# Optimization experiments

Hardware: AMD Instinct MI355X
Metric: run time of the kernel (lower is better)

Reference implementation:

```python
import jax, jax.numpy as jnp
import numpy as np

N_NODES, N_EDGES, HIDDEN, N_GRAPHS = 100000, 500000, 128, 2048
ATOM_DIM, BOND_DIM, OUT_DIM = 4, 3, 1


def setup_inputs() -> dict:
    key = jax.random.key(0)
    ks = jax.random.split(key, 13)
    s = 0.05  # small init scale to keep relu+scatter depth iterations numerically tame
    return {
        "x": jax.random.normal(ks[0], (N_NODES, ATOM_DIM), jnp.float32),
        "edge_index": jax.random.randint(ks[1], (2, N_EDGES), 0, N_NODES, dtype=jnp.int32),
        "edge_attr": jax.random.normal(ks[2], (N_EDGES, BOND_DIM), jnp.float32),
        "batch": jnp.sort(jax.random.randint(ks[3], (N_NODES,), 0, N_GRAPHS, dtype=jnp.int32)),
        "depth": 3,
        # DMPNN weights (bias=False)
        "W_i": jax.random.normal(ks[4], (HIDDEN, ATOM_DIM + BOND_DIM), jnp.float32) * s,
        "W_m": jax.random.normal(ks[5], (HIDDEN, HIDDEN), jnp.float32) * s,
        "W_a": jax.random.normal(ks[6], (HIDDEN, ATOM_DIM + HIDDEN), jnp.float32) * s,
        # FFN: Linear(d,4d) -> relu -> dropout(eval=identity) -> Linear(4d,d)
        "W1": jax.random.normal(ks[7], (4 * HIDDEN, HIDDEN), jnp.float32) * s,
        "b1": jnp.zeros((4 * HIDDEN,), jnp.float32),
        "W2": jax.random.normal(ks[8], (HIDDEN, 4 * HIDDEN), jnp.float32) * s,
        "b2": jnp.zeros((HIDDEN,), jnp.float32),
        "W_last": jax.random.normal(ks[9], (OUT_DIM, HIDDEN), jnp.float32) * s,
        "b_last": jnp.zeros((OUT_DIM,), jnp.float32),
    }


def reference(x, edge_index, edge_attr, batch, depth, W_i, W_m, W_a, W1, b1, W2, b2, W_last, b_last):
    src, dst = edge_index[0], edge_index[1]
    E = edge_attr.shape[0]
    N = x.shape[0]
    # h: per-edge state [E, H]
    h = jax.nn.relu(jnp.concatenate([x[src], edge_attr], axis=1) @ W_i.T)
    for _ in range(depth):
        # message: relu(W_m h) gathered at src, scatter-add to dst; PyG infers
        # dim_size from h (edge-level here), so aggregation buffer has E rows.
        m = jax.nn.relu(h @ W_m.T)
        h = h + jax.ops.segment_sum(m[src], dst, num_segments=E)
    # index_add_ edge states to nodes
    node_emb = jax.ops.segment_sum(h, dst, num_segments=N)  # [N, H]
    node_emb = jax.nn.relu(jnp.concatenate([x, node_emb], axis=1) @ W_a.T)
    # global_add_pool over graphs
    g = jax.ops.segment_sum(node_emb, batch, num_segments=N_GRAPHS)  # [G, H]
    g = jax.nn.relu(g @ W1.T + b1) @ W2.T + b2  # FFN (dropout eval = identity)
    return g @ W_last.T + b_last  # [G, OUT_DIM]
```

## Files before the change

kernel.cpp:

```cpp
#include <hip/hip_runtime.h>


#define NN 100000
#define NE 500000
#define HID 128
#define NG 2048
#define NB_SCAN 391

typedef __attribute__((ext_vector_type(8))) short bf16x8;
typedef __attribute__((ext_vector_type(4))) float f32x4;

__device__ __forceinline__ float b2f(ushort u) {
  return __uint_as_float(((uint)u) << 16);
}
__device__ __forceinline__ ushort f2b(float f) {
  uint u = __float_as_uint(f);
  return (ushort)((u + 0x7FFF + ((u >> 16) & 1)) >> 16);
}

__global__ __launch_bounds__(256) void k_convw(const float* __restrict__ Wm,
    const float* __restrict__ Wa, ushort* __restrict__ wmb, ushort* __restrict__ wab) {
  int i = blockIdx.x * 256 + threadIdx.x;
  if (i >= HID * HID) return;
  wmb[i] = f2b(Wm[i]);
  int c = i >> 7, k = i & 127;
  wab[i] = f2b(Wa[c * 132 + 4 + k]);
}

__global__ __launch_bounds__(256) void k_init_h(const int* __restrict__ src,
    const float* __restrict__ x, const float* __restrict__ ea,
    const float* __restrict__ Wi, ushort* __restrict__ h) {
  __shared__ float wis[HID * 7];
  for (int i = threadIdx.x; i < HID * 7; i += 256) wis[i] = Wi[i];
  __syncthreads();
  int idx = blockIdx.x * 256 + threadIdx.x;
  int e = idx >> 7, c = idx & 127;
  if (e >= NN) return;
  int s = src[e];
  const float* w = &wis[c * 7];
  float acc = x[s*4+0]*w[0] + x[s*4+1]*w[1] + x[s*4+2]*w[2] + x[s*4+3]*w[3]
            + ea[e*3+0]*w[4] + ea[e*3+1]*w[5] + ea[e*3+2]*w[6];
  h[(size_t)e * HID + c] = f2b(fmaxf(acc, 0.f));
}

__global__ __launch_bounds__(256) void k_hist(const int* __restrict__ dst,
                                              int* __restrict__ cnt) {
  int e = blockIdx.x * 256 + threadIdx.x;
  if (e < NE) atomicAdd(&cnt[dst[e]], 1);
}

__global__ __launch_bounds__(256) void k_scan1(const int* __restrict__ cnt,
    int* __restrict__ outp, int* __restrict__ bsums) {
  __shared__ int s[256];
  int t = threadIdx.x;
  int i = blockIdx.x * 256 + t;
  int v = (i < NN) ? cnt[i] : 0;
  s[t] = v;
  __syncthreads();
  for (int off = 1; off < 256; off <<= 1) {
    int u = (t >= off) ? s[t - off] : 0;
    __syncthreads();
    s[t] += u;
    __syncthreads();
  }
  if (i < NN) outp[i] = s[t] - v;
  if (t == 255) bsums[blockIdx.x] = s[255];
}

__global__ __launch_bounds__(512) void k_scan2(int* __restrict__ bsums) {
  __shared__ int s[512];
  int t = threadIdx.x;
  int v = (t < NB_SCAN) ? bsums[t] : 0;
  s[t] = v;
  __syncthreads();
  for (int off = 1; off < 512; off <<= 1) {
    int u = (t >= off) ? s[t - off] : 0;
    __syncthreads();
    s[t] += u;
    __syncthreads();
  }
  if (t < NB_SCAN) bsums[t] = s[t] - v;
}

__global__ __launch_bounds__(256) void k_scan3(int* __restrict__ outp,
                                               const int* __restrict__ bsums) {
  int i = blockIdx.x * 256 + threadIdx.x;
  if (i < NN) outp[i] += bsums[blockIdx.x];
  if (i == 0) outp[NN] = NE;
}

__global__ __launch_bounds__(256) void k_fill(const int* __restrict__ src,
    const int* __restrict__ dst, const int* __restrict__ rowptr,
    int* __restrict__ cursor, int* __restrict__ csr_src, int* __restrict__ csr_eid) {
  int e = blockIdx.x * 256 + threadIdx.x;
  if (e >= NE) return;
  int d = dst[e];
  int pos = atomicAdd(&cursor[d], 1);
  int o = rowptr[d] + pos;
  csr_src[o] = src[e];
  csr_eid[o] = e;
}

__global__ __launch_bounds__(256) void k_goff(const int* __restrict__ batch,
                                              int* __restrict__ goff) {
  int g = blockIdx.x * 256 + threadIdx.x;
  if (g > NG) return;
  int lo = 0, hi = NN;
  while (lo < hi) { int mid = (lo + hi) >> 1; if (batch[mid] < g) lo = mid + 1; else hi = mid; }
  goff[g] = lo;
}

template <bool HASX>
__global__ __launch_bounds__(256) void k_mfma(const ushort* __restrict__ A,
    const ushort* __restrict__ Wb, const float* __restrict__ X,
    const float* __restrict__ WaF, ushort* __restrict__ O, int nrows) {
  int tid = threadIdx.x;
  int wave = tid >> 6;
  int lane = tid & 63;
  int wr = wave >> 1, wc = wave & 1;
  int row0 = blockIdx.x * 64 + wr * 32;
  int col0 = wc * 64;
  int l15 = lane & 15, l4 = lane >> 4;

  f32x4 acc[2][4];
#pragma unroll
  for (int mi = 0; mi < 2; ++mi)
#pragma unroll
    for (int ni = 0; ni < 4; ++ni) acc[mi][ni] = (f32x4){0.f, 0.f, 0.f, 0.f};

  if (HASX) {
    float4 wv[4];
#pragma unroll
    for (int ni = 0; ni < 4; ++ni)
      wv[ni] = *reinterpret_cast<const float4*>(&WaF[(size_t)(col0 + ni * 16 + l15) * 132]);
#pragma unroll
    for (int mi = 0; mi < 2; ++mi)
#pragma unroll
      for (int j = 0; j < 4; ++j) {
        int r = row0 + mi * 16 + l4 * 4 + j;
        if (r < nrows) {
          float4 xv = *reinterpret_cast<const float4*>(&X[(size_t)r * 4]);
#pragma unroll
          for (int ni = 0; ni < 4; ++ni)
            acc[mi][ni][j] = xv.x * wv[ni].x + xv.y * wv[ni].y
                           + xv.z * wv[ni].z + xv.w * wv[ni].w;
        }
      }
  }

  const bf16x8 zero8 = {0, 0, 0, 0, 0, 0, 0, 0};
#pragma unroll
  for (int k0 = 0; k0 < HID; k0 += 32) {
    bf16x8 a[2], b[4];
#pragma unroll
    for (int mi = 0; mi < 2; ++mi) {
      int r = row0 + mi * 16 + l15;
      a[mi] = (r < nrows)
            ? *reinterpret_cast<const bf16x8*>(&A[(size_t)r * HID + k0 + l4 * 8])
            : zero8;
    }
#pragma unroll
    for (int ni = 0; ni < 4; ++ni) {
      int c = col0 + ni * 16 + l15;
      b[ni] = *reinterpret_cast<const bf16x8*>(&Wb[(size_t)c * HID + k0 + l4 * 8]);
    }
#pragma unroll
    for (int mi = 0; mi < 2; ++mi)
#pragma unroll
      for (int ni = 0; ni < 4; ++ni)
        acc[mi][ni] = __builtin_amdgcn_mfma_f32_16x16x32_bf16(a[mi], b[ni], acc[mi][ni], 0, 0, 0);
  }

#pragma unroll
  for (int mi = 0; mi < 2; ++mi)
#pragma unroll
    for (int j = 0; j < 4; ++j) {
      int r = row0 + mi * 16 + l4 * 4 + j;
      if (r >= nrows) continue;
#pragma unroll
      for (int ni = 0; ni < 4; ++ni) {
        int c = col0 + ni * 16 + l15;
        O[(size_t)r * HID + c] = f2b(fmaxf(acc[mi][ni][j], 0.f));
      }
    }
}

__global__ __launch_bounds__(256) void k_gather_add(const ushort* __restrict__ m,
    const int* __restrict__ rowptr, const int* __restrict__ csr_src,
    ushort* __restrict__ h) {
  int idx = blockIdx.x * 256 + threadIdx.x;
  int n = idx >> 5;
  if (n >= NN) return;
  int c4 = (idx & 31) << 2;
  int beg = rowptr[n], end = rowptr[n + 1];
  float a0 = 0.f, a1 = 0.f, a2 = 0.f, a3 = 0.f;
  for (int i = beg; i < end; ++i) {
    int s = csr_src[i];
    ushort4 v = *reinterpret_cast<const ushort4*>(&m[(size_t)s * HID + c4]);
    a0 += b2f(v.x); a1 += b2f(v.y); a2 += b2f(v.z); a3 += b2f(v.w);
  }
  ushort* p = &h[(size_t)n * HID + c4];
  ushort4 hv = *reinterpret_cast<const ushort4*>(p);
  ushort4 o;
  o.x = f2b(b2f(hv.x) + a0); o.y = f2b(b2f(hv.y) + a1);
  o.z = f2b(b2f(hv.z) + a2); o.w = f2b(b2f(hv.w) + a3);
  *reinterpret_cast<ushort4*>(p) = o;
}

__global__ __launch_bounds__(256) void k_node_agg(const ushort* __restrict__ h,
    const int* __restrict__ rowptr, const int* __restrict__ csr_src,
    const int* __restrict__ csr_eid, const float* __restrict__ x,
    const float* __restrict__ ea, const float* __restrict__ Wi,
    ushort* __restrict__ ne) {
  int idx = blockIdx.x * 256 + threadIdx.x;
  int n = idx >> 5;
  int c4 = (idx & 31) << 2;
  float w[4][7];
#pragma unroll
  for (int j = 0; j < 4; ++j)
#pragma unroll
    for (int k = 0; k < 7; ++k) w[j][k] = Wi[(c4 + j) * 7 + k];
  if (n >= NN) return;
  int beg = rowptr[n], end = rowptr[n + 1];
  float a0 = 0.f, a1 = 0.f, a2 = 0.f, a3 = 0.f;
  for (int i = beg; i < end; ++i) {
    int e = csr_eid[i];
    if (e < NN) {
      ushort4 v = *reinterpret_cast<const ushort4*>(&h[(size_t)e * HID + c4]);
      a0 += b2f(v.x); a1 += b2f(v.y); a2 += b2f(v.z); a3 += b2f(v.w);
    } else {
      int s = csr_src[i];
      float4 xv = *reinterpret_cast<const float4*>(&x[(size_t)s * 4]);
      float e0 = ea[(size_t)e*3+0], e1 = ea[(size_t)e*3+1], e2 = ea[(size_t)e*3+2];
      a0 += fmaxf(xv.x*w[0][0]+xv.y*w[0][1]+xv.z*w[0][2]+xv.w*w[0][3]+e0*w[0][4]+e1*w[0][5]+e2*w[0][6], 0.f);
      a1 += fmaxf(xv.x*w[1][0]+xv.y*w[1][1]+xv.z*w[1][2]+xv.w*w[1][3]+e0*w[1][4]+e1*w[1][5]+e2*w[1][6], 0.f);
      a2 += fmaxf(xv.x*w[2][0]+xv.y*w[2][1]+xv.z*w[2][2]+xv.w*w[2][3]+e0*w[2][4]+e1*w[2][5]+e2*w[2][6], 0.f);
      a3 += fmaxf(xv.x*w[3][0]+xv.y*w[3][1]+xv.z*w[3][2]+xv.w*w[3][3]+e0*w[3][4]+e1*w[3][5]+e2*w[3][6], 0.f);
    }
  }
  ushort4 o;
  o.x = f2b(a0); o.y = f2b(a1); o.z = f2b(a2); o.w = f2b(a3);
  *reinterpret_cast<ushort4*>(&ne[(size_t)n * HID + c4]) = o;
}

__global__ __launch_bounds__(256) void k_pool(const ushort* __restrict__ na,
    const int* __restrict__ goff, float* __restrict__ g) {
  int idx = blockIdx.x * 256 + threadIdx.x;
  int gid = idx >> 5;
  if (gid >= NG) return;
  int c4 = (idx & 31) << 2;
  int beg = goff[gid], end = goff[gid + 1];
  float a0 = 0.f, a1 = 0.f, a2 = 0.f, a3 = 0.f;
  for (int n = beg; n < end; ++n) {
    ushort4 v = *reinterpret_cast<const ushort4*>(&na[(size_t)n * HID + c4]);
    a0 += b2f(v.x); a1 += b2f(v.y); a2 += b2f(v.z); a3 += b2f(v.w);
  }
  *reinterpret_cast<float4*>(&g[(size_t)gid * HID + c4]) = make_float4(a0, a1, a2, a3);
}

template <bool RELU>
__global__ __launch_bounds__(256) void k_gemm64(const float* __restrict__ A,
    const float* __restrict__ W, const float* __restrict__ bias,
    float* __restrict__ O, int nrows, int K, int N) {
  __shared__ float As[64][33];
  __shared__ float Bs[32][68];
  int tid = threadIdx.x;
  int row0 = blockIdx.x * 64;
  int col0 = blockIdx.y * 64;
  int tn = tid & 15;
  int tm = tid >> 4;
  float acc[4][4];
#pragma unroll
  for (int i = 0; i < 4; ++i)
#pragma unroll
    for (int j = 0; j < 4; ++j) acc[i][j] = 0.f;

  for (int k0 = 0; k0 < K; k0 += 32) {
    int ar = tid >> 3;
    int ak = (tid & 7) << 2;
#pragma unroll
    for (int rr = 0; rr < 2; ++rr) {
      int r = row0 + ar + rr * 32;
      float4 v = make_float4(0.f, 0.f, 0.f, 0.f);
      if (r < nrows) v = *reinterpret_cast<const float4*>(&A[(size_t)r * K + k0 + ak]);
      As[ar + rr*32][ak+0] = v.x; As[ar + rr*32][ak+1] = v.y;
      As[ar + rr*32][ak+2] = v.z; As[ar + rr*32][ak+3] = v.w;
    }
    int c = tid & 63;
    int kq = tid >> 6;
#pragma unroll
    for (int it = 0; it < 2; ++it) {
      int kk = kq * 4 + it * 16;
      float4 v = *reinterpret_cast<const float4*>(&W[(size_t)(col0 + c) * K + k0 + kk]);
      Bs[kk+0][c] = v.x; Bs[kk+1][c] = v.y; Bs[kk+2][c] = v.z; Bs[kk+3][c] = v.w;
    }
    __syncthreads();
#pragma unroll 8
    for (int k = 0; k < 32; ++k) {
      float av[4];
#pragma unroll
      for (int i = 0; i < 4; ++i) av[i] = As[tm*4 + i][k];
      float4 bv = *reinterpret_cast<const float4*>(&Bs[k][tn*4]);
#pragma unroll
      for (int i = 0; i < 4; ++i) {
        acc[i][0] = fmaf(av[i], bv.x, acc[i][0]);
        acc[i][1] = fmaf(av[i], bv.y, acc[i][1]);
        acc[i][2] = fmaf(av[i], bv.z, acc[i][2]);
        acc[i][3] = fmaf(av[i], bv.w, acc[i][3]);
      }
    }
    __syncthreads();
  }
#pragma unroll
  for (int i = 0; i < 4; ++i) {
    int r = row0 + tm * 4 + i;
    if (r >= nrows) continue;
    float4 o;
    int c = col0 + tn * 4;
    o.x = acc[i][0] + bias[c+0];
    o.y = acc[i][1] + bias[c+1];
    o.z = acc[i][2] + bias[c+2];
    o.w = acc[i][3] + bias[c+3];
    if (RELU) {
      o.x = fmaxf(o.x, 0.f); o.y = fmaxf(o.y, 0.f);
      o.z = fmaxf(o.z, 0.f); o.w = fmaxf(o.w, 0.f);
    }
    *reinterpret_cast<float4*>(&O[(size_t)r * N + c]) = o;
  }
}

__global__ __launch_bounds__(256) void k_last(const float* __restrict__ g3,
    const float* __restrict__ Wl, const float* __restrict__ bl,
    float* __restrict__ out) {
  int wid = (blockIdx.x * 256 + threadIdx.x) >> 6;
  int lane = threadIdx.x & 63;
  if (wid >= NG) return;
  float a = g3[(size_t)wid*128 + lane] * Wl[lane]
          + g3[(size_t)wid*128 + 64 + lane] * Wl[64 + lane];
  for (int off = 32; off; off >>= 1) a += __shfl_down(a, off);
  if (lane == 0) out[wid] = a + bl[0];
}

extern "C" void kernel_launch(void* const* d_in, const int* in_sizes, int n_in,
                              void* d_out, int out_size, void* d_ws, size_t ws_size,
                              hipStream_t stream) {
  const float* x    = (const float*)d_in[0];
  const int*   eidx = (const int*)d_in[1];
  const float* ea   = (const float*)d_in[2];
  const int*   batch= (const int*)d_in[3];
  const float* Wi   = (const float*)d_in[5];
  const float* Wm   = (const float*)d_in[6];
  const float* Wa   = (const float*)d_in[7];
  const float* W1   = (const float*)d_in[8];
  const float* b1   = (const float*)d_in[9];
  const float* W2   = (const float*)d_in[10];
  const float* b2   = (const float*)d_in[11];
  const float* Wl   = (const float*)d_in[12];
  const float* bl   = (const float*)d_in[13];
  float* out = (float*)d_out;

  const int* src = eidx;
  const int* dst = eidx + NE;

  char* p = (char*)d_ws;
  ushort* hb  = (ushort*)p; p += (size_t)NN * HID * 2;
  ushort* mb  = (ushort*)p; p += (size_t)NN * HID * 2;
  ushort* wmb = (ushort*)p; p += (size_t)HID * HID * 2;
  ushort* wab = (ushort*)p; p += (size_t)HID * HID * 2;
  float* g  = (float*)p; p += (size_t)NG * 128 * 4;
  float* g2 = (float*)p; p += (size_t)NG * 512 * 4;
  float* g3 = (float*)p; p += (size_t)NG * 128 * 4;
  int* rowptr = (int*)p; p += (size_t)(NN + 4) * 4;
  int* cursor = (int*)p; p += (size_t)NN * 4;
  int* bsums  = (int*)p; p += 512 * 4;
  int* goff   = (int*)p; p += (size_t)(NG + 4) * 4;
  int* csr_src= (int*)p; p += (size_t)NE * 4;
  int* csr_eid= (int*)p; p += (size_t)NE * 4;

  hipMemsetAsync(rowptr, 0, (size_t)(NN + 4 + NN) * sizeof(int), stream);
  k_hist <<<(NE + 255) / 256, 256, 0, stream>>>(dst, rowptr);
  k_scan1<<<NB_SCAN, 256, 0, stream>>>(rowptr, cursor, bsums);
  k_scan2<<<1, 512, 0, stream>>>(bsums);
  k_scan3<<<NB_SCAN, 256, 0, stream>>>(cursor, bsums);
  int* rp  = cursor;
  int* cur = rowptr;
  hipMemsetAsync(cur, 0, (size_t)NN * sizeof(int), stream);
  k_fill <<<(NE + 255) / 256, 256, 0, stream>>>(src, dst, rp, cur, csr_src, csr_eid);
  k_goff <<<(NG + 256) / 256, 256, 0, stream>>>(batch, goff);

  k_convw<<<(HID * HID + 255) / 256, 256, 0, stream>>>(Wm, Wa, wmb, wab);

  k_init_h<<<(NN * HID) / 256, 256, 0, stream>>>(src, x, ea, Wi, hb);

  int gemm_grid = (NN + 63) / 64;
  for (int it = 0; it < 3; ++it) {
    k_mfma<false><<<gemm_grid, 256, 0, stream>>>(hb, wmb, nullptr, nullptr, mb, NN);
    k_gather_add<<<(NN * 32 + 255) / 256, 256, 0, stream>>>(mb, rp, csr_src, hb);
  }

  k_node_agg<<<(NN * 32 + 255) / 256, 256, 0, stream>>>(hb, rp, csr_src, csr_eid,
                                                        x, ea, Wi, mb);
  k_mfma<true><<<gemm_grid, 256, 0, stream>>>(mb, wab, x, Wa, hb, NN);

  k_pool<<<(NG * 32 + 255) / 256, 256, 0, stream>>>(hb, goff, g);

  dim3 grid1((NG + 63) / 64, 512 / 64);
  k_gemm64<true><<<grid1, 256, 0, stream>>>(g, W1, b1, g2, NG, 128, 512);
  dim3 grid2((NG + 63) / 64, 128 / 64);
  k_gemm64<false><<<grid2, 256, 0, stream>>>(g2, W2, b2, g3, NG, 512, 128);
  k_last<<<(NG * 64) / 256, 256, 0, stream>>>(g3, Wl, bl, out);
}
```

Baseline: 502.9 us.

## Fuse gather-add into MFMA GEMM via LDS staging and pack CSR as int2

The scatter/gather-add of each depth iteration is fused with the next W_m GEMM: each block gathers neighbour messages for its 64 rows, updates h, writes the bf16 tile into swizzled LDS and feeds the MFMA from LDS. The same is done for node aggregation followed by the W_a GEMM. Message buffers are ping-ponged, and the CSR src/eid arrays are interleaved into one int2 array. Gather and pool kernels now use 8-wide bf16 vectors per thread. The aim is fewer launches and no separate h round-trip to global memory between gather and GEMM. In exchange, the gather phase gets less parallelism per block, which may expose latency.

```diff
diff --git a/kernel.cpp b/kernel.cpp
--- a/kernel.cpp
+++ b/kernel.cpp
@@ -16,6 +16,16 @@
 __device__ __forceinline__ ushort f2b(float f) {
   uint u = __float_as_uint(f);
   return (ushort)((u + 0x7FFF + ((u >> 16) & 1)) >> 16);
+}
+__device__ __forceinline__ void acc8(float* a, bf16x8 v) {
+#pragma unroll
+  for (int j = 0; j < 8; ++j) a[j] += b2f((ushort)v[j]);
+}
+__device__ __forceinline__ bf16x8 pack8(const float* a) {
+  bf16x8 o;
+#pragma unroll
+  for (int j = 0; j < 8; ++j) o[j] = (short)f2b(a[j]);
+  return o;
 }
 
 __global__ __launch_bounds__(256) void k_convw(const float* __restrict__ Wm,
@@ -91,14 +101,12 @@
 
 __global__ __launch_bounds__(256) void k_fill(const int* __restrict__ src,
     const int* __restrict__ dst, const int* __restrict__ rowptr,
-    int* __restrict__ cursor, int* __restrict__ csr_src, int* __restrict__ csr_eid) {
+    int* __restrict__ cursor, int2* __restrict__ csr) {
   int e = blockIdx.x * 256 + threadIdx.x;
   if (e >= NE) return;
   int d = dst[e];
   int pos = atomicAdd(&cursor[d], 1);
-  int o = rowptr[d] + pos;
-  csr_src[o] = src[e];
-  csr_eid[o] = e;
+  csr[rowptr[d] + pos] = make_int2(src[e], e);
 }
 
 __global__ __launch_bounds__(256) void k_goff(const int* __restrict__ batch,
@@ -110,60 +118,174 @@
   goff[g] = lo;
 }
 
-template <bool HASX>
-__global__ __launch_bounds__(256) void k_mfma(const ushort* __restrict__ A,
-    const ushort* __restrict__ Wb, const float* __restrict__ X,
-    const float* __restrict__ WaF, ushort* __restrict__ O, int nrows) {
+template <bool GATHER>
+__global__ __launch_bounds__(256) void k_fused(const ushort* __restrict__ Asrc,
+    const ushort* __restrict__ Wb, const int* __restrict__ rowptr,
+    const int2* __restrict__ csr, ushort* __restrict__ h_io,
+    ushort* __restrict__ O) {
+  __shared__ ulong2 As_q[1024];
+  char* lds = (char*)As_q;
   int tid = threadIdx.x;
-  int wave = tid >> 6;
-  int lane = tid & 63;
+  int row0 = blockIdx.x * 64;
+
+  if (GATHER) {
+    int g = tid >> 4, l = tid & 15, c8 = l * 8;
+    for (int nn = g; nn < 64; nn += 16) {
+      int n = row0 + nn;
+      uint off = ((uint)nn * 256 + (uint)c8 * 2) ^ ((nn & 7) << 4);
+      if (n < NN) {
+        float a[8];
+        bf16x8 hv = *reinterpret_cast<const bf16x8*>(&h_io[(size_t)n * HID + c8]);
+#pragma unroll
+        for (int j = 0; j < 8; ++j) a[j] = b2f((ushort)hv[j]);
+        int beg = rowptr[n], end = rowptr[n + 1];
+        for (int i = beg; i < end; ++i) {
+          int s = csr[i].x;
+          acc8(a, *reinterpret_cast<const bf16x8*>(&Asrc[(size_t)s * HID + c8]));
+        }
+        bf16x8 o = pack8(a);
+        *reinterpret_cast<bf16x8*>(&h_io[(size_t)n * HID + c8]) = o;
+        *reinterpret_cast<bf16x8*>(lds + off) = o;
+      } else {
+        *reinterpret_cast<bf16x8*>(lds + off) = (bf16x8){0,0,0,0,0,0,0,0};
+      }
+    }
+  } else {
+    for (int t = tid; t < 1024; t += 256) {
+      int nn = t >> 4, ck = t & 15;
+      int n = row0 + nn;
+      bf16x8 v = (n < NN)
+        ? *reinterpret_cast<const bf16x8*>(&Asrc[(size_t)n * HID + ck * 8])
+        : (bf16x8){0,0,0,0,0,0,0,0};
+      uint off = ((uint)nn * 256 + (uint)ck * 16) ^ ((nn & 7) << 4);
+      *reinterpret_cast<bf16x8*>(lds + off) = v;
+    }
+  }
+  __syncthreads();
+
+  int wave = tid >> 6, lane = tid & 63;
   int wr = wave >> 1, wc = wave & 1;
-  int row0 = blockIdx.x * 64 + wr * 32;
-  int col0 = wc * 64;
   int l15 = lane & 15, l4 = lane >> 4;
-
+  int lr0 = wr * 32, col0 = wc * 64;
   f32x4 acc[2][4];
 #pragma unroll
   for (int mi = 0; mi < 2; ++mi)
 #pragma unroll
     for (int ni = 0; ni < 4; ++ni) acc[mi][ni] = (f32x4){0.f, 0.f, 0.f, 0.f};
 
-  if (HASX) {
-    float4 wv[4];
+#pragma unroll
+  for (int k0 = 0; k0 < HID; k0 += 32) {
+    bf16x8 a[2], b[4];
+#pragma unroll
+    for (int mi = 0; mi < 2; ++mi) {
+      int rr = lr0 + mi * 16 + l15;
+      uint off = ((uint)rr * 256 + (uint)(k0 + l4 * 8) * 2) ^ ((rr & 7) << 4);
+      a[mi] = *reinterpret_cast<const bf16x8*>(lds + off);
+    }
 #pragma unroll
     for (int ni = 0; ni < 4; ++ni)
-      wv[ni] = *reinterpret_cast<const float4*>(&WaF[(size_t)(col0 + ni * 16 + l15) * 132]);
+      b[ni] = *reinterpret_cast<const bf16x8*>(&Wb[(size_t)(col0 + ni*16 + l15) * HID + k0 + l4*8]);
 #pragma unroll
     for (int mi = 0; mi < 2; ++mi)
 #pragma unroll
-      for (int j = 0; j < 4; ++j) {
-        int r = row0 + mi * 16 + l4 * 4 + j;
-        if (r < nrows) {
-          float4 xv = *reinterpret_cast<const float4*>(&X[(size_t)r * 4]);
-#pragma unroll
-          for (int ni = 0; ni < 4; ++ni)
-            acc[mi][ni][j] = xv.x * wv[ni].x + xv.y * wv[ni].y
-                           + xv.z * wv[ni].z + xv.w * wv[ni].w;
+      for (int ni = 0; ni < 4; ++ni)
+        acc[mi][ni] = __builtin_amdgcn_mfma_f32_16x16x32_bf16(a[mi], b[ni], acc[mi][ni], 0, 0, 0);
+  }
+
+#pragma unroll
+  for (int mi = 0; mi < 2; ++mi)
+#pragma unroll
+    for (int j = 0; j < 4; ++j) {
+      int r = row0 + lr0 + mi * 16 + l4 * 4 + j;
+      if (r >= NN) continue;
+#pragma unroll
+      for (int ni = 0; ni < 4; ++ni)
+        O[(size_t)r * HID + col0 + ni * 16 + l15] = f2b(fmaxf(acc[mi][ni][j], 0.f));
+    }
+}
+
+__global__ __launch_bounds__(256) void k_fused_agg(const ushort* __restrict__ h,
+    const int* __restrict__ rowptr, const int2* __restrict__ csr,
+    const float* __restrict__ x, const float* __restrict__ ea,
+    const float* __restrict__ Wi, const ushort* __restrict__ Wab,
+    const float* __restrict__ WaF, ushort* __restrict__ O) {
+  __shared__ ulong2 As_q[1024];
+  char* lds = (char*)As_q;
+  int tid = threadIdx.x;
+  int row0 = blockIdx.x * 64;
+
+  int g = tid >> 4, l = tid & 15, c8 = l * 8;
+  float w[8][7];
+#pragma unroll
+  for (int j = 0; j < 8; ++j)
+#pragma unroll
+    for (int k = 0; k < 7; ++k) w[j][k] = Wi[(c8 + j) * 7 + k];
+
+  for (int nn = g; nn < 64; nn += 16) {
+    int n = row0 + nn;
+    uint off = ((uint)nn * 256 + (uint)c8 * 2) ^ ((nn & 7) << 4);
+    if (n < NN) {
+      float a[8];
+#pragma unroll
+      for (int j = 0; j < 8; ++j) a[j] = 0.f;
+      int beg = rowptr[n], end = rowptr[n + 1];
+      for (int i = beg; i < end; ++i) {
+        int2 se = csr[i];
+        int e = se.y;
+        if (e < NN) {
+          acc8(a, *reinterpret_cast<const bf16x8*>(&h[(size_t)e * HID + c8]));
+        } else {
+          int s = se.x;
+          float4 xv = *reinterpret_cast<const float4*>(&x[(size_t)s * 4]);
+          float e0 = ea[(size_t)e*3+0], e1 = ea[(size_t)e*3+1], e2 = ea[(size_t)e*3+2];
+#pragma unroll
+          for (int j = 0; j < 8; ++j)
+            a[j] += fmaxf(xv.x*w[j][0] + xv.y*w[j][1] + xv.z*w[j][2] + xv.w*w[j][3]
+                        + e0*w[j][4] + e1*w[j][5] + e2*w[j][6], 0.f);
         }
       }
-  }
-
-  const bf16x8 zero8 = {0, 0, 0, 0, 0, 0, 0, 0};
+      *reinterpret_cast<bf16x8*>(lds + off) = pack8(a);
+    } else {
+      *reinterpret_cast<bf16x8*>(lds + off) = (bf16x8){0,0,0,0,0,0,0,0};
+    }
+  }
+  __syncthreads();
+
+  int wave = tid >> 6, lane = tid & 63;
+  int wr = wave >> 1, wc = wave & 1;
+  int l15 = lane & 15, l4 = lane >> 4;
+  int lr0 = wr * 32, col0 = wc * 64;
+  f32x4 acc[2][4];
+  {
+    float4 wv[4];
+#pragma unroll
+    for (int ni = 0; ni < 4; ++ni)
+      wv[ni] = *reinterpret_cast<const float4*>(&WaF[(size_t)(col0 + ni*16 + l15) * 132]);
+#pragma unroll
+    for (int mi = 0; mi < 2; ++mi)
+#pragma unroll
+      for (int j = 0; j < 4; ++j) {
+        int r = row0 + lr0 + mi * 16 + l4 * 4 + j;
+        float4 xv = (r < NN) ? *reinterpret_cast<const float4*>(&x[(size_t)r * 4])
+                             : make_float4(0.f, 0.f, 0.f, 0.f);
+#pragma unroll
+        for (int ni = 0; ni < 4; ++ni)
+          acc[mi][ni][j] = xv.x*wv[ni].x + xv.y*wv[ni].y + xv.z*wv[ni].z + xv.w*wv[ni].w;
+      }
+  }
+
 #pragma unroll
   for (int k0 = 0; k0 < HID; k0 += 32) {
     bf16x8 a[2], b[4];
 #pragma unroll
     for (int mi = 0; mi < 2; ++mi) {
-      int r = row0 + mi * 16 + l15;
-      a[mi] = (r < nrows)
-            ? *reinterpret_cast<const bf16x8*>(&A[(size_t)r * HID + k0 + l4 * 8])
-            : zero8;
-    }
-#pragma unroll
-    for (int ni = 0; ni < 4; ++ni) {
-      int c = col0 + ni * 16 + l15;
-      b[ni] = *reinterpret_cast<const bf16x8*>(&Wb[(size_t)c * HID + k0 + l4 * 8]);
-    }
+      int rr = lr0 + mi * 16 + l15;
+      uint off = ((uint)rr * 256 + (uint)(k0 + l4 * 8) * 2) ^ ((rr & 7) << 4);
+      a[mi] = *reinterpret_cast<const bf16x8*>(lds + off);
+    }
+#pragma unroll
+    for (int ni = 0; ni < 4; ++ni)
+      b[ni] = *reinterpret_cast<const bf16x8*>(&Wab[(size_t)(col0 + ni*16 + l15) * HID + k0 + l4*8]);
 #pragma unroll
     for (int mi = 0; mi < 2; ++mi)
 #pragma unroll
@@ -175,87 +297,47 @@
   for (int mi = 0; mi < 2; ++mi)
 #pragma unroll
     for (int j = 0; j < 4; ++j) {
-      int r = row0 + mi * 16 + l4 * 4 + j;
-      if (r >= nrows) continue;
-#pragma unroll
-      for (int ni = 0; ni < 4; ++ni) {
-        int c = col0 + ni * 16 + l15;
-        O[(size_t)r * HID + c] = f2b(fmaxf(acc[mi][ni][j], 0.f));
-      }
-    }
-}
-
-__global__ __launch_bounds__(256) void k_gather_add(const ushort* __restrict__ m,
-    const int* __restrict__ rowptr, const int* __restrict__ csr_src,
+      int r = row0 + lr0 + mi * 16 + l4 * 4 + j;
+      if (r >= NN) continue;
+#pragma unroll
+      for (int ni = 0; ni < 4; ++ni)
+        O[(size_t)r * HID + col0 + ni * 16 + l15] = f2b(fmaxf(acc[mi][ni][j], 0.f));
+    }
+}
+
+__global__ __launch_bounds__(256) void k_gather16(const ushort* __restrict__ m,
+    const int* __restrict__ rowptr, const int2* __restrict__ csr,
     ushort* __restrict__ h) {
   int idx = blockIdx.x * 256 + threadIdx.x;
-  int n = idx >> 5;
+  int n = idx >> 4;
   if (n >= NN) return;
-  int c4 = (idx & 31) << 2;
+  int c8 = (idx & 15) * 8;
+  float a[8];
+  bf16x8 hv = *reinterpret_cast<const bf16x8*>(&h[(size_t)n * HID + c8]);
+#pragma unroll
+  for (int j = 0; j < 8; ++j) a[j] = b2f((ushort)hv[j]);
   int beg = rowptr[n], end = rowptr[n + 1];
-  float a0 = 0.f, a1 = 0.f, a2 = 0.f, a3 = 0.f;
   for (int i = beg; i < end; ++i) {
-    int s = csr_src[i];
-    ushort4 v = *reinterpret_cast<const ushort4*>(&m[(size_t)s * HID + c4]);
-    a0 += b2f(v.x); a1 += b2f(v.y); a2 += b2f(v.z); a3 += b2f(v.w);
-  }
-  ushort* p = &h[(size_t)n * HID + c4];
-  ushort4 hv = *reinterpret_cast<const ushort4*>(p);
-  ushort4 o;
-  o.x = f2b(b2f(hv.x) + a0); o.y = f2b(b2f(hv.y) + a1);
-  o.z = f2b(b2f(hv.z) + a2); o.w = f2b(b2f(hv.w) + a3);
-  *reinterpret_cast<ushort4*>(p) = o;
-}
-
-__global__ __launch_bounds__(256) void k_node_agg(const ushort* __restrict__ h,
-    const int* __restrict__ rowptr, const int* __restrict__ csr_src,
-    const int* __restrict__ csr_eid, const float* __restrict__ x,
-    const float* __restrict__ ea, const float* __restrict__ Wi,
-    ushort* __restrict__ ne) {
-  int idx = blockIdx.x * 256 + threadIdx.x;
-  int n = idx >> 5;
-  int c4 = (idx & 31) << 2;
-  float w[4][7];
-#pragma unroll
-  for (int j = 0; j < 4; ++j)
-#pragma unroll
-    for (int k = 0; k < 7; ++k) w[j][k] = Wi[(c4 + j) * 7 + k];
-  if (n >= NN) return;
-  int beg = rowptr[n], end = rowptr[n + 1];
-  float a0 = 0.f, a1 = 0.f, a2 = 0.f, a3 = 0.f;
-  for (int i = beg; i < end; ++i) {
-    int e = csr_eid[i];
-    if (e < NN) {
-      ushort4 v = *reinterpret_cast<const ushort4*>(&h[(size_t)e * HID + c4]);
-      a0 += b2f(v.x); a1 += b2f(v.y); a2 += b2f(v.z); a3 += b2f(v.w);
-    } else {
-      int s = csr_src[i];
-      float4 xv = *reinterpret_cast<const float4*>(&x[(size_t)s * 4]);
-      float e0 = ea[(size_t)e*3+0], e1 = ea[(size_t)e*3+1], e2 = ea[(size_t)e*3+2];
-      a0 += fmaxf(xv.x*w[0][0]+xv.y*w[0][1]+xv.z*w[0][2]+xv.w*w[0][3]+e0*w[0][4]+e1*w[0][5]+e2*w[0][6], 0.f);
-      a1 += fmaxf(xv.x*w[1][0]+xv.y*w[1][1]+xv.z*w[1][2]+xv.w*w[1][3]+e0*w[1][4]+e1*w[1][5]+e2*w[1][6], 0.f);
-      a2 += fmaxf(xv.x*w[2][0]+xv.y*w[2][1]+xv.z*w[2][2]+xv.w*w[2][3]+e0*w[2][4]+e1*w[2][5]+e2*w[2][6], 0.f);
-      a3 += fmaxf(xv.x*w[3][0]+xv.y*w[3][1]+xv.z*w[3][2]+xv.w*w[3][3]+e0*w[3][4]+e1*w[3][5]+e2*w[3][6], 0.f);
-    }
-  }
-  ushort4 o;
-  o.x = f2b(a0); o.y = f2b(a1); o.z = f2b(a2); o.w = f2b(a3);
-  *reinterpret_cast<ushort4*>(&ne[(size_t)n * HID + c4]) = o;
+    int s = csr[i].x;
+    acc8(a, *reinterpret_cast<const bf16x8*>(&m[(size_t)s * HID + c8]));
+  }
+  *reinterpret_cast<bf16x8*>(&h[(size_t)n * HID + c8]) = pack8(a);
 }
 
 __global__ __launch_bounds__(256) void k_pool(const ushort* __restrict__ na,
     const int* __restrict__ goff, float* __restrict__ g) {
   int idx = blockIdx.x * 256 + threadIdx.x;
-  int gid = idx >> 5;
+  int gid = idx >> 4;
   if (gid >= NG) return;
-  int c4 = (idx & 31) << 2;
+  int c8 = (idx & 15) * 8;
   int beg = goff[gid], end = goff[gid + 1];
-  float a0 = 0.f, a1 = 0.f, a2 = 0.f, a3 = 0.f;
-  for (int n = beg; n < end; ++n) {
-    ushort4 v = *reinterpret_cast<const ushort4*>(&na[(size_t)n * HID + c4]);
-    a0 += b2f(v.x); a1 += b2f(v.y); a2 += b2f(v.z); a3 += b2f(v.w);
-  }
-  *reinterpret_cast<float4*>(&g[(size_t)gid * HID + c4]) = make_float4(a0, a1, a2, a3);
+  float a[8];
+#pragma unroll
+  for (int j = 0; j < 8; ++j) a[j] = 0.f;
+  for (int n = beg; n < end; ++n)
+    acc8(a, *reinterpret_cast<const bf16x8*>(&na[(size_t)n * HID + c8]));
+  *reinterpret_cast<float4*>(&g[(size_t)gid * HID + c8]) = make_float4(a[0], a[1], a[2], a[3]);
+  *reinterpret_cast<float4*>(&g[(size_t)gid * HID + c8 + 4]) = make_float4(a[4], a[5], a[6], a[7]);
 }
 
 template <bool RELU>
@@ -364,18 +446,18 @@
 
   char* p = (char*)d_ws;
   ushort* hb  = (ushort*)p; p += (size_t)NN * HID * 2;
-  ushort* mb  = (ushort*)p; p += (size_t)NN * HID * 2;
+  ushort* mA  = (ushort*)p; p += (size_t)NN * HID * 2;
+  ushort* mB  = (ushort*)p; p += (size_t)NN * HID * 2;
   ushort* wmb = (ushort*)p; p += (size_t)HID * HID * 2;
   ushort* wab = (ushort*)p; p += (size_t)HID * HID * 2;
   float* g  = (float*)p; p += (size_t)NG * 128 * 4;
   float* g2 = (float*)p; p += (size_t)NG * 512 * 4;
   float* g3 = (float*)p; p += (size_t)NG * 128 * 4;
+  int2* csr   = (int2*)p; p += (size_t)NE * 8;
   int* rowptr = (int*)p; p += (size_t)(NN + 4) * 4;
   int* cursor = (int*)p; p += (size_t)NN * 4;
   int* bsums  = (int*)p; p += 512 * 4;
   int* goff   = (int*)p; p += (size_t)(NG + 4) * 4;
-  int* csr_src= (int*)p; p += (size_t)NE * 4;
-  int* csr_eid= (int*)p; p += (size_t)NE * 4;
 
   hipMemsetAsync(rowptr, 0, (size_t)(NN + 4 + NN) * sizeof(int), stream);
   k_hist <<<(NE + 255) / 256, 256, 0, stream>>>(dst, rowptr);
@@ -385,24 +467,21 @@
   int* rp  = cursor;
   int* cur = rowptr;
   hipMemsetAsync(cur, 0, (size_t)NN * sizeof(int), stream);
-  k_fill <<<(NE + 255) / 256, 256, 0, stream>>>(src, dst, rp, cur, csr_src, csr_eid);
+  k_fill <<<(NE + 255) / 256, 256, 0, stream>>>(src, dst, rp, cur, csr);
   k_goff <<<(NG + 256) / 256, 256, 0, stream>>>(batch, goff);
 
   k_convw<<<(HID * HID + 255) / 256, 256, 0, stream>>>(Wm, Wa, wmb, wab);
 
   k_init_h<<<(NN * HID) / 256, 256, 0, stream>>>(src, x, ea, Wi, hb);
 
-  int gemm_grid = (NN + 63) / 64;
-  for (int it = 0; it < 3; ++it) {
-    k_mfma<false><<<gemm_grid, 256, 0, stream>>>(hb, wmb, nullptr, nullptr, mb, NN);
-    k_gather_add<<<(NN * 32 + 255) / 256, 256, 0, stream>>>(mb, rp, csr_src, hb);
-  }
-
-  k_node_agg<<<(NN * 32 + 255) / 256, 256, 0, stream>>>(hb, rp, csr_src, csr_eid,
-                                                        x, ea, Wi, mb);
-  k_mfma<true><<<gemm_grid, 256, 0, stream>>>(mb, wab, x, Wa, hb, NN);
-
-  k_pool<<<(NG * 32 + 255) / 256, 256, 0, stream>>>(hb, goff, g);
+  int fgrid = (NN + 63) / 64;
+  k_fused<false><<<fgrid, 256, 0, stream>>>(hb, wmb, nullptr, nullptr, nullptr, mA);
+  k_fused<true ><<<fgrid, 256, 0, stream>>>(mA, wmb, rp, csr, hb, mB);
+  k_fused<true ><<<fgrid, 256, 0, stream>>>(mB, wmb, rp, csr, hb, mA);
+  k_gather16<<<(NN * 16 + 255) / 256, 256, 0, stream>>>(mA, rp, csr, hb);
+  k_fused_agg<<<fgrid, 256, 0, stream>>>(hb, rp, csr, x, ea, Wi, wab, Wa, mB);
+
+  k_pool<<<(NG * 16 + 255) / 256, 256, 0, stream>>>(mB, goff, g);
 
   dim3 grid1((NG + 63) / 64, 512 / 64);
   k_gemm64<true><<<grid1, 256, 0, stream>>>(g, W1, b1, g2, NG, 128, 512);
```

Measured after the change: 494.8 us. About the same (-1.6%).

## Partition CSR by edge class and widen gather kernels to 8-wide bf16 loads

Applied to the files above, without the earlier changes.

The CSR fill now splits each node's incoming edges into two groups: edges with id below NN, whose stored state is read, and the remaining edges, whose initial state is recomputed. This removes the per-edge branch in node aggregation. The gather, node-aggregation and pooling kernels now use 16 threads per row with 16-byte bf16x8 loads and unrolled 4-way neighbour loops, which gives more loads in flight and fewer threads. The cost is an extra histogram counter, an extra midpoint kernel and more registers per thread (8x7 weights in node_agg).

```diff
diff --git a/kernel.cpp b/kernel.cpp
--- a/kernel.cpp
+++ b/kernel.cpp
@@ -16,6 +16,16 @@
 __device__ __forceinline__ ushort f2b(float f) {
   uint u = __float_as_uint(f);
   return (ushort)((u + 0x7FFF + ((u >> 16) & 1)) >> 16);
+}
+__device__ __forceinline__ void acc8(float* a, bf16x8 v) {
+#pragma unroll
+  for (int j = 0; j < 8; ++j) a[j] += b2f((ushort)v[j]);
+}
+__device__ __forceinline__ bf16x8 pack8(const float* a) {
+  bf16x8 o;
+#pragma unroll
+  for (int j = 0; j < 8; ++j) o[j] = (short)f2b(a[j]);
+  return o;
 }
 
 __global__ __launch_bounds__(256) void k_convw(const float* __restrict__ Wm,
@@ -43,10 +53,13 @@
   h[(size_t)e * HID + c] = f2b(fmaxf(acc, 0.f));
 }
 
-__global__ __launch_bounds__(256) void k_hist(const int* __restrict__ dst,
-                                              int* __restrict__ cnt) {
+__global__ __launch_bounds__(256) void k_hist2(const int* __restrict__ dst,
+    int* __restrict__ cnt, int* __restrict__ cnt_lo) {
   int e = blockIdx.x * 256 + threadIdx.x;
-  if (e < NE) atomicAdd(&cnt[dst[e]], 1);
+  if (e >= NE) return;
+  int d = dst[e];
+  atomicAdd(&cnt[d], 1);
+  if (e < NN) atomicAdd(&cnt_lo[d], 1);
 }
 
 __global__ __launch_bounds__(256) void k_scan1(const int* __restrict__ cnt,
@@ -89,14 +102,22 @@
   if (i == 0) outp[NN] = NE;
 }
 
-__global__ __launch_bounds__(256) void k_fill(const int* __restrict__ src,
+__global__ __launch_bounds__(256) void k_mid(const int* __restrict__ rowptr,
+    const int* __restrict__ cnt_lo, int* __restrict__ midp) {
+  int i = blockIdx.x * 256 + threadIdx.x;
+  if (i < NN) midp[i] = rowptr[i] + cnt_lo[i];
+}
+
+__global__ __launch_bounds__(256) void k_fill2(const int* __restrict__ src,
     const int* __restrict__ dst, const int* __restrict__ rowptr,
-    int* __restrict__ cursor, int* __restrict__ csr_src, int* __restrict__ csr_eid) {
+    const int* __restrict__ midp, int* __restrict__ cur_lo,
+    int* __restrict__ cur_hi, int* __restrict__ csr_src, int* __restrict__ csr_eid) {
   int e = blockIdx.x * 256 + threadIdx.x;
   if (e >= NE) return;
   int d = dst[e];
-  int pos = atomicAdd(&cursor[d], 1);
-  int o = rowptr[d] + pos;
+  int o;
+  if (e < NN) o = rowptr[d] + atomicAdd(&cur_lo[d], 1);
+  else        o = midp[d]   + atomicAdd(&cur_hi[d], 1);
   csr_src[o] = src[e];
   csr_eid[o] = e;
 }
@@ -185,77 +206,110 @@
     }
 }
 
-__global__ __launch_bounds__(256) void k_gather_add(const ushort* __restrict__ m,
+__global__ __launch_bounds__(256) void k_gather4(const ushort* __restrict__ m,
     const int* __restrict__ rowptr, const int* __restrict__ csr_src,
     ushort* __restrict__ h) {
   int idx = blockIdx.x * 256 + threadIdx.x;
-  int n = idx >> 5;
+  int n = idx >> 4;
   if (n >= NN) return;
-  int c4 = (idx & 31) << 2;
+  int c8 = (idx & 15) * 8;
+  float a[8];
+  bf16x8 hv = *reinterpret_cast<const bf16x8*>(&h[(size_t)n * HID + c8]);
+#pragma unroll
+  for (int j = 0; j < 8; ++j) a[j] = b2f((ushort)hv[j]);
   int beg = rowptr[n], end = rowptr[n + 1];
-  float a0 = 0.f, a1 = 0.f, a2 = 0.f, a3 = 0.f;
-  for (int i = beg; i < end; ++i) {
+  int i = beg;
+  for (; i + 4 <= end; i += 4) {
+    int s0 = csr_src[i+0], s1 = csr_src[i+1], s2 = csr_src[i+2], s3 = csr_src[i+3];
+    bf16x8 v0 = *reinterpret_cast<const bf16x8*>(&m[(size_t)s0 * HID + c8]);
+    bf16x8 v1 = *reinterpret_cast<const bf16x8*>(&m[(size_t)s1 * HID + c8]);
+    bf16x8 v2 = *reinterpret_cast<const bf16x8*>(&m[(size_t)s2 * HID + c8]);
+    bf16x8 v3 = *reinterpret_cast<const bf16x8*>(&m[(size_t)s3 * HID + c8]);
+    acc8(a, v0); acc8(a, v1); acc8(a, v2); acc8(a, v3);
+  }
+  for (; i < end; ++i) {
     int s = csr_src[i];
-    ushort4 v = *reinterpret_cast<const ushort4*>(&m[(size_t)s * HID + c4]);
-    a0 += b2f(v.x); a1 += b2f(v.y); a2 += b2f(v.z); a3 += b2f(v.w);
-  }
-  ushort* p = &h[(size_t)n * HID + c4];
-  ushort4 hv = *reinterpret_cast<const ushort4*>(p);
-  ushort4 o;
-  o.x = f2b(b2f(hv.x) + a0); o.y = f2b(b2f(hv.y) + a1);
-  o.z = f2b(b2f(hv.z) + a2); o.w = f2b(b2f(hv.w) + a3);
-  *reinterpret_cast<ushort4*>(p) = o;
-}
-
-__global__ __launch_bounds__(256) void k_node_agg(const ushort* __restrict__ h,
-    const int* __restrict__ rowptr, const int* __restrict__ csr_src,
-    const int* __restrict__ csr_eid, const float* __restrict__ x,
-    const float* __restrict__ ea, const float* __restrict__ Wi,
-    ushort* __restrict__ ne) {
+    acc8(a, *reinterpret_cast<const bf16x8*>(&m[(size_t)s * HID + c8]));
+  }
+  *reinterpret_cast<bf16x8*>(&h[(size_t)n * HID + c8]) = pack8(a);
+}
+
+__device__ __forceinline__ void h0acc(float* a, const float w[8][7],
+                                      float4 xv, float e0, float e1, float e2) {
+#pragma unroll
+  for (int j = 0; j < 8; ++j) {
+    float t = xv.x*w[j][0] + xv.y*w[j][1] + xv.z*w[j][2] + xv.w*w[j][3]
+            + e0*w[j][4] + e1*w[j][5] + e2*w[j][6];
+    a[j] += fmaxf(t, 0.f);
+  }
+}
+
+__global__ __launch_bounds__(256) void k_node_agg2(const ushort* __restrict__ h,
+    const int* __restrict__ rowptr, const int* __restrict__ midp,
+    const int* __restrict__ csr_src, const int* __restrict__ csr_eid,
+    const float* __restrict__ x, const float* __restrict__ ea,
+    const float* __restrict__ Wi, ushort* __restrict__ ne) {
   int idx = blockIdx.x * 256 + threadIdx.x;
-  int n = idx >> 5;
-  int c4 = (idx & 31) << 2;
-  float w[4][7];
-#pragma unroll
-  for (int j = 0; j < 4; ++j)
-#pragma unroll
-    for (int k = 0; k < 7; ++k) w[j][k] = Wi[(c4 + j) * 7 + k];
+  int n = idx >> 4;
+  int c8 = (idx & 15) * 8;
+  float w[8][7];
+#pragma unroll
+  for (int j = 0; j < 8; ++j)
+#pragma unroll
+    for (int k = 0; k < 7; ++k) w[j][k] = Wi[(c8 + j) * 7 + k];
   if (n >= NN) return;
-  int beg = rowptr[n], end = rowptr[n + 1];
-  float a0 = 0.f, a1 = 0.f, a2 = 0.f, a3 = 0.f;
-  for (int i = beg; i < end; ++i) {
+  int beg = rowptr[n], mid = midp[n], end = rowptr[n + 1];
+  float a[8];
+#pragma unroll
+  for (int j = 0; j < 8; ++j) a[j] = 0.f;
+
+  int i = beg;
+  for (; i + 4 <= mid; i += 4) {
+    int e0 = csr_eid[i+0], e1 = csr_eid[i+1], e2 = csr_eid[i+2], e3 = csr_eid[i+3];
+    bf16x8 v0 = *reinterpret_cast<const bf16x8*>(&h[(size_t)e0 * HID + c8]);
+    bf16x8 v1 = *reinterpret_cast<const bf16x8*>(&h[(size_t)e1 * HID + c8]);
+    bf16x8 v2 = *reinterpret_cast<const bf16x8*>(&h[(size_t)e2 * HID + c8]);
+    bf16x8 v3 = *reinterpret_cast<const bf16x8*>(&h[(size_t)e3 * HID + c8]);
+    acc8(a, v0); acc8(a, v1); acc8(a, v2); acc8(a, v3);
+  }
+  for (; i < mid; ++i) {
     int e = csr_eid[i];
-    if (e < NN) {
-      ushort4 v = *reinterpret_cast<const ushort4*>(&h[(size_t)e * HID + c4]);
-      a0 += b2f(v.x); a1 += b2f(v.y); a2 += b2f(v.z); a3 += b2f(v.w);
-    } else {
-      int s = csr_src[i];
-      float4 xv = *reinterpret_cast<const float4*>(&x[(size_t)s * 4]);
-      float e0 = ea[(size_t)e*3+0], e1 = ea[(size_t)e*3+1], e2 = ea[(size_t)e*3+2];
-      a0 += fmaxf(xv.x*w[0][0]+xv.y*w[0][1]+xv.z*w[0][2]+xv.w*w[0][3]+e0*w[0][4]+e1*w[0][5]+e2*w[0][6], 0.f);
-      a1 += fmaxf(xv.x*w[1][0]+xv.y*w[1][1]+xv.z*w[1][2]+xv.w*w[1][3]+e0*w[1][4]+e1*w[1][5]+e2*w[1][6], 0.f);
-      a2 += fmaxf(xv.x*w[2][0]+xv.y*w[2][1]+xv.z*w[2][2]+xv.w*w[2][3]+e0*w[2][4]+e1*w[2][5]+e2*w[2][6], 0.f);
-      a3 += fmaxf(xv.x*w[3][0]+xv.y*w[3][1]+xv.z*w[3][2]+xv.w*w[3][3]+e0*w[3][4]+e1*w[3][5]+e2*w[3][6], 0.f);
-    }
-  }
-  ushort4 o;
-  o.x = f2b(a0); o.y = f2b(a1); o.z = f2b(a2); o.w = f2b(a3);
-  *reinterpret_cast<ushort4*>(&ne[(size_t)n * HID + c4]) = o;
+    acc8(a, *reinterpret_cast<const bf16x8*>(&h[(size_t)e * HID + c8]));
+  }
+
+  i = mid;
+  for (; i + 2 <= end; i += 2) {
+    int s0 = csr_src[i+0], e0 = csr_eid[i+0];
+    int s1 = csr_src[i+1], e1 = csr_eid[i+1];
+    float4 xv0 = *reinterpret_cast<const float4*>(&x[(size_t)s0 * 4]);
+    float4 xv1 = *reinterpret_cast<const float4*>(&x[(size_t)s1 * 4]);
+    float a00 = ea[(size_t)e0*3+0], a01 = ea[(size_t)e0*3+1], a02 = ea[(size_t)e0*3+2];
+    float a10 = ea[(size_t)e1*3+0], a11 = ea[(size_t)e1*3+1], a12 = ea[(size_t)e1*3+2];
+    h0acc(a, w, xv0, a00, a01, a02);
+    h0acc(a, w, xv1, a10, a11, a12);
+  }
+  for (; i < end; ++i) {
+    int s = csr_src[i], e = csr_eid[i];
+    float4 xv = *reinterpret_cast<const float4*>(&x[(size_t)s * 4]);
+    h0acc(a, w, xv, ea[(size_t)e*3+0], ea[(size_t)e*3+1], ea[(size_t)e*3+2]);
+  }
+  *reinterpret_cast<bf16x8*>(&ne[(size_t)n * HID + c8]) = pack8(a);
 }
 
 __global__ __launch_bounds__(256) void k_pool(const ushort* __restrict__ na,
     const int* __restrict__ goff, float* __restrict__ g) {
   int idx = blockIdx.x * 256 + threadIdx.x;
-  int gid = idx >> 5;
+  int gid = idx >> 4;
   if (gid >= NG) return;
-  int c4 = (idx & 31) << 2;
+  int c8 = (idx & 15) * 8;
   int beg = goff[gid], end = goff[gid + 1];
-  float a0 = 0.f, a1 = 0.f, a2 = 0.f, a3 = 0.f;
-  for (int n = beg; n < end; ++n) {
-    ushort4 v = *reinterpret_cast<const ushort4*>(&na[(size_t)n * HID + c4]);
-    a0 += b2f(v.x); a1 += b2f(v.y); a2 += b2f(v.z); a3 += b2f(v.w);
-  }
-  *reinterpret_cast<float4*>(&g[(size_t)gid * HID + c4]) = make_float4(a0, a1, a2, a3);
+  float a[8];
+#pragma unroll
+  for (int j = 0; j < 8; ++j) a[j] = 0.f;
+  for (int n = beg; n < end; ++n)
+    acc8(a, *reinterpret_cast<const bf16x8*>(&na[(size_t)n * HID + c8]));
+  *reinterpret_cast<float4*>(&g[(size_t)gid * HID + c8]) = make_float4(a[0], a[1], a[2], a[3]);
+  *reinterpret_cast<float4*>(&g[(size_t)gid * HID + c8 + 4]) = make_float4(a[4], a[5], a[6], a[7]);
 }
 
 template <bool RELU>
@@ -370,39 +424,43 @@
   float* g  = (float*)p; p += (size_t)NG * 128 * 4;
   float* g2 = (float*)p; p += (size_t)NG * 512 * 4;
   float* g3 = (float*)p; p += (size_t)NG * 128 * 4;
+  int* csr_src = (int*)p; p += (size_t)NE * 4;
+  int* csr_eid = (int*)p; p += (size_t)NE * 4;
+  int* cnt    = (int*)p; p += (size_t)NN * 4;
+  int* cnt_lo = (int*)p; p += (size_t)NN * 4;
+  int* cur_lo = (int*)p; p += (size_t)NN * 4;
+  int* cur_hi = (int*)p; p += (size_t)NN * 4;
   int* rowptr = (int*)p; p += (size_t)(NN + 4) * 4;
-  int* cursor = (int*)p; p += (size_t)NN * 4;
+  int* midp   = (int*)p; p += (size_t)NN * 4;
   int* bsums  = (int*)p; p += 512 * 4;
   int* goff   = (int*)p; p += (size_t)(NG + 4) * 4;
-  int* csr_src= (int*)p; p += (size_t)NE * 4;
-  int* csr_eid= (int*)p; p += (size_t)NE * 4;
-
-  hipMemsetAsync(rowptr, 0, (size_t)(NN + 4 + NN) * sizeof(int), stream);
-  k_hist <<<(NE + 255) / 256, 256, 0, stream>>>(dst, rowptr);
-  k_scan1<<<NB_SCAN, 256, 0, stream>>>(rowptr, cursor, bsums);
+
+  hipMemsetAsync(cnt, 0, (size_t)4 * NN * sizeof(int), stream);
+  k_hist2<<<(NE + 255) / 256, 256, 0, stream>>>(dst, cnt, cnt_lo);
+  k_scan1<<<NB_SCAN, 256, 0, stream>>>(cnt, rowptr, bsums);
   k_scan2<<<1, 512, 0, stream>>>(bsums);
-  k_scan3<<<NB_SCAN, 256, 0, stream>>>(cursor, bsums);
-  int* rp  = cursor;
-  int* cur = rowptr;
-  hipMemsetAsync(cur, 0, (size_t)NN * sizeof(int), stream);
-  k_fill <<<(NE + 255) / 256, 256, 0, stream>>>(src, dst, rp, cur, csr_src, csr_eid);
+  k_scan3<<<NB_SCAN, 256, 0, stream>>>(rowptr, bsums);
+  k_mid  <<<NB_SCAN, 256, 0, stream>>>(rowptr, cnt_lo, midp);
+  k_fill2<<<(NE + 255) / 256, 256, 0, stream>>>(src, dst, rowptr, midp,
+                                                cur_lo, cur_hi, csr_src, csr_eid);
   k_goff <<<(NG + 256) / 256, 256, 0, stream>>>(batch, goff);
 
   k_convw<<<(HID * HID + 255) / 256, 256, 0, stream>>>(Wm, Wa, wmb, wab);
 
   k_init_h<<<(NN * HID) / 256, 256, 0, stream>>>(src, x, ea, Wi, hb);
 
-  int gemm_grid = (NN + 63) / 64;
+  int ggrid = (NN + 63) / 64;
+  int sgrid = (NN * 16 + 255) / 256;
   for (int it = 0; it < 3; ++it) {
-    k_mfma<false><<<gemm_grid, 256, 0, stream>>>(hb, wmb, nullptr, nullptr, mb, NN);
-    k_gather_add<<<(NN * 32 + 255) / 256, 256, 0, stream>>>(mb, rp, csr_src, hb);
-  }
-
-  k_node_agg<<<(NN * 32 + 255) / 256, 256, 0, stream>>>(hb, rp, csr_src, csr_eid,
-                                                        x, ea, Wi, mb);
-  k_mfma<true><<<gemm_grid, 256, 0, stream>>>(mb, wab, x, Wa, hb, NN);
-
-  k_pool<<<(NG * 32 + 255) / 256, 256, 0, stream>>>(hb, goff, g);
+    k_mfma<false><<<ggrid, 256, 0, stream>>>(hb, wmb, nullptr, nullptr, mb, NN);
+    k_gather4<<<sgrid, 256, 0, stream>>>(mb, rowptr, csr_src, hb);
+  }
+
+  k_node_agg2<<<sgrid, 256, 0, stream>>>(hb, rowptr, midp, csr_src, csr_eid,
+                                         x, ea, Wi, mb);
+  k_mfma<true><<<ggrid, 256, 0, stream>>>(mb, wab, x, Wa, hb, NN);
+
+  k_pool<<<(NG * 16 + 255) / 256, 256, 0, stream>>>(hb, goff, g);
 
   dim3 grid1((NG + 63) / 64, 512 / 64);
   k_gemm64<true><<<grid1, 256, 0, stream>>>(g, W1, b1, g2, NG, 128, 512);
```

After: 455.6 us. 1.1x faster.
